# Kernel tuning notes

Measured on AMD Instinct MI355X. Metric: run time of the kernel, lower is better.

The kernel has to match this reference:

```python
import jax, jax.numpy as jnp
import numpy as np

NUM_HEADS = 8
QK_DIM = 64
V_DIM = 64


def _conv1x1(W, b, x):
    # W: [out, in], x: [N, in, T, V] -> [N, out, T, V]
    return jnp.einsum('oc,nctv->notv', W, x) + b[None, :, None, None]


def setup_inputs() -> dict:
    key = jax.random.key(0)
    ks = jax.random.split(key, 10)
    N, C, T, V = 8, 256, 1024, 25
    s = 0.02
    return {
        'feature': jax.random.normal(ks[0], (N, C, T, V), jnp.float32),
        'text_feature': jax.random.normal(ks[1], (1, 512, 1, V), jnp.float32),
        'Wq': jax.random.normal(ks[2], (NUM_HEADS * QK_DIM, 512), jnp.float32) * s,
        'bq': jax.random.normal(ks[3], (NUM_HEADS * QK_DIM,), jnp.float32) * s,
        'Wk': jax.random.normal(ks[4], (NUM_HEADS * QK_DIM, 512), jnp.float32) * s,
        'bk': jax.random.normal(ks[5], (NUM_HEADS * QK_DIM,), jnp.float32) * s,
        'Wv': jax.random.normal(ks[6], (V_DIM, C), jnp.float32) * s,
        'bv': jax.random.normal(ks[7], (V_DIM,), jnp.float32) * s,
        'Wo': jax.random.normal(ks[8], (C, NUM_HEADS * V_DIM), jnp.float32) * s,
        'bo': jax.random.normal(ks[9], (C,), jnp.float32) * s,
    }


def reference(feature, text_feature, Wq, bq, Wk, bk, Wv, bv, Wo, bo):
    N, C, T, V = feature.shape
    tf = jnp.broadcast_to(text_feature, (N, 512, 1, V))  # expand over batch
    # Q/K from text features (T dim collapses to 1)
    q = _conv1x1(Wq, bq, tf).reshape(N, NUM_HEADS, QK_DIM, V)
    k = _conv1x1(Wk, bk, tf).reshape(N, NUM_HEADS, QK_DIM, V)
    v = _conv1x1(Wv, bv, feature)  # [N, v_dim, T, V]
    energy = jnp.einsum('nhcu,nhcv->nhuv', q, k) / jnp.sqrt(jnp.float32(QK_DIM))
    attn = jax.nn.softmax(energy, axis=-1)  # [N, H, V, V]
    z = jnp.einsum('nctu,nhuv->nhctv', v, attn).reshape(N, NUM_HEADS * V_DIM, T, V)
    out = _conv1x1(Wo, bo, z) + feature
    return out
```

## Files before the change

kernel.cpp:

```cpp
#include <hip/hip_runtime.h>
#include <hip/hip_bf16.h>


typedef __attribute__((ext_vector_type(8))) short short8;
typedef __attribute__((ext_vector_type(4))) float f4v;

static __device__ __forceinline__ unsigned short f2bf(float f) {
  union { float f; unsigned u; } v; v.f = f;
  unsigned r = v.u + 0x7fffu + ((v.u >> 16) & 1u);
  return (unsigned short)(r >> 16);
}
static __device__ __forceinline__ float bf2f(unsigned short h) {
  union { unsigned u; float f; } v; v.u = ((unsigned)h) << 16;
  return v.f;
}


__global__ void k_qk_conv(const float* __restrict__ tf,
                          const float* __restrict__ Wq, const float* __restrict__ bq,
                          const float* __restrict__ Wk, const float* __restrict__ bk,
                          const float* __restrict__ Wv, const float* __restrict__ Wo,
                          unsigned short* __restrict__ WvP,
                          unsigned short* __restrict__ WoP,
                          float* __restrict__ qkP)
{
  __shared__ float tfl[12800];
  const int b = blockIdx.x, tid = threadIdx.x;
  if (b < 100) {
    for (int i = tid; i < 12800; i += 256) tfl[i] = tf[i];
    __syncthreads();
    int idx = b * 256 + tid;
    int isK = idx >= 12800;
    int j = isK ? idx - 12800 : idx;
    int g = j / 25, u = j - 25 * g;
    const float* wrow = (isK ? Wk : Wq) + g * 512;
    float s = (isK ? bk : bq)[g];
    for (int i = 0; i < 512; ++i) s += wrow[i] * tfl[i * 25 + u];
    qkP[idx] = s;
  } else {
    int cb = b - 100;
    for (int i = cb * 256 + tid; i < 16896; i += 64 * 256) {
      int c = i / 264, kk = i - 264 * c;
      WvP[i] = (kk < 256) ? f2bf(Wv[c * 256 + kk]) : (unsigned short)0;
    }
    for (int i = cb * 256 + tid; i < 147456; i += 64 * 256) {
      int hh = i / 18432, rr = i - 18432 * hh;
      int o = rr / 72, kk = rr - 72 * o;
      WoP[i] = (kk < 64) ? f2bf(Wo[o * 512 + hh * 64 + kk]) : (unsigned short)0;
    }
  }
}

__global__ void k_attn(const float* __restrict__ qkP,
                       unsigned short* __restrict__ attnP)
{
  __shared__ float ql[1600], kl[1600], attl[625];
  const int h = blockIdx.x, tid = threadIdx.x;
  for (int i = tid; i < 1600; i += 256) {
    ql[i] = qkP[h * 1600 + i];
    kl[i] = qkP[12800 + h * 1600 + i];
  }
  __syncthreads();
  if (tid < 25) {
    int u = tid;
    float e[25];
    float mx = -1e30f;
    #pragma unroll
    for (int v = 0; v < 25; ++v) {
      float s = 0.f;
      #pragma unroll
      for (int r = 0; r < 64; ++r) s += ql[r * 25 + u] * kl[r * 25 + v];
      s *= 0.125f;
      e[v] = s;
      mx = fmaxf(mx, s);
    }
    float den = 0.f;
    #pragma unroll
    for (int v = 0; v < 25; ++v) { e[v] = __expf(e[v] - mx); den += e[v]; }
    float inv = 1.f / den;
    #pragma unroll
    for (int v = 0; v < 25; ++v) attl[u * 25 + v] = e[v] * inv;
  }
  __syncthreads();
  for (int i = tid; i < 1280; i += 256) {
    int vp = i / 40, u = i - 40 * vp;
    attnP[h * 1280 + i] =
        (vp < 25 && u < 25) ? f2bf(attl[u * 25 + vp]) : (unsigned short)0;
  }
}

__launch_bounds__(512, 2)
__global__ void k_main(const float* __restrict__ feature,
                       const float* __restrict__ bv,
                       const float* __restrict__ bo,
                       const unsigned short* __restrict__ WvP,
                       const unsigned short* __restrict__ WoP,
                       const unsigned short* __restrict__ attnP,
                       float* __restrict__ out)
{
  extern __shared__ char smem[];
  unsigned short* Fl = (unsigned short*)smem;
  unsigned short* Vl = (unsigned short*)(smem + 67584);
  unsigned short* Zl = (unsigned short*)(smem + 84992);
  unsigned short* Wl = (unsigned short*)(smem + 103424);

  const int tid  = threadIdx.x;
  const int wave = tid >> 6;
  const int lane = tid & 63;
  const int quad = lane >> 4;
  const int l16  = lane & 15;
  const int n  = blockIdx.x >> 8;
  const int tb = blockIdx.x & 255;
  const int t0 = tb * 4;

  {
    short8 z = {0, 0, 0, 0, 0, 0, 0, 0};
    short8* fz = (short8*)smem;
    for (int i = tid; i < 4224; i += 512) fz[i] = z;
  }
  __syncthreads();

  {
    const int c = tid >> 1, p = tid & 1;
    const float4* src = reinterpret_cast<const float4*>(
        feature + ((size_t)(n * 256 + c) * 1024 + t0) * 25);
    for (int i = p; i < 25; i += 2) {
      float4 f = src[i];
      float vv[4] = {f.x, f.y, f.z, f.w};
      int j0 = 4 * i;
      #pragma unroll
      for (int e = 0; e < 4; ++e) {
        int j = j0 + e;
        int t = j / 25;
        int vp = j - 25 * t;
        Fl[(t * 32 + vp) * 264 + c] = f2bf(vv[e]);
      }
    }
  }
  __syncthreads();

  const int wm = wave >> 1, wn = wave & 1;

  f4v acc[4][4];
  #pragma unroll
  for (int mi = 0; mi < 4; ++mi) {
    #pragma unroll
    for (int r = 0; r < 4; ++r) {
      int o = wm * 64 + mi * 16 + quad * 4 + r;
      float bor = bo[o];
      #pragma unroll
      for (int ni = 0; ni < 4; ++ni) {
        int colb = wn * 64 + ni * 16 + l16;
        acc[mi][ni][r] = bor + bf2f(Fl[colb * 264 + o]);
      }
    }
  }

  {
    const int mt1 = wave & 3, nh1 = wave >> 2;
    f4v accv[4];
    #pragma unroll
    for (int ni = 0; ni < 4; ++ni) {
      #pragma unroll
      for (int r = 0; r < 4; ++r) accv[ni][r] = bv[mt1 * 16 + quad * 4 + r];
    }
    #pragma unroll
    for (int ks = 0; ks < 8; ++ks) {
      short8 a = *reinterpret_cast<const short8*>(
          WvP + (mt1 * 16 + l16) * 264 + ks * 32 + quad * 8);
      #pragma unroll
      for (int ni = 0; ni < 4; ++ni) {
        int colb = (4 * nh1 + ni) * 16 + l16;
        short8 b = *reinterpret_cast<const short8*>(
            &Fl[colb * 264 + ks * 32 + quad * 8]);
        accv[ni] = __builtin_amdgcn_mfma_f32_16x16x32_bf16(a, b, accv[ni], 0, 0, 0);
      }
    }
    #pragma unroll
    for (int ni = 0; ni < 4; ++ni) {
      int colb = (4 * nh1 + ni) * 16 + l16;
      #pragma unroll
      for (int r = 0; r < 4; ++r) {
        int c = mt1 * 16 + quad * 4 + r;
        Vl[c * 136 + colb] = f2bf(accv[ni][r]);
      }
    }
  }
  __syncthreads();

  #pragma unroll 1
  for (int h = 0; h < 8; ++h) {
    const short8* wsrc = reinterpret_cast<const short8*>(WoP + h * 18432);
    short8 wo_stage[5];
    #pragma unroll
    for (int c2 = 0; c2 < 5; ++c2) {
      int i = tid + c2 * 512;
      if (i < 2304) wo_stage[c2] = wsrc[i];
    }

    {
      const int t2 = wave >> 1, mh = wave & 1;
      f4v accz[2][2];
      #pragma unroll
      for (int m2 = 0; m2 < 2; ++m2) {
        #pragma unroll
        for (int n2 = 0; n2 < 2; ++n2) {
          f4v z = {0.f, 0.f, 0.f, 0.f};
          accz[m2][n2] = z;
        }
      }
      short8 bfrag[2];
      #pragma unroll
      for (int n2 = 0; n2 < 2; ++n2)
        bfrag[n2] = *reinterpret_cast<const short8*>(
            attnP + h * 1280 + (n2 * 16 + l16) * 40 + quad * 8);
      #pragma unroll
      for (int m2 = 0; m2 < 2; ++m2) {
        short8 a = *reinterpret_cast<const short8*>(
            &Vl[((2 * mh + m2) * 16 + l16) * 136 + t2 * 32 + quad * 8]);
        #pragma unroll
        for (int n2 = 0; n2 < 2; ++n2)
          accz[m2][n2] =
              __builtin_amdgcn_mfma_f32_16x16x32_bf16(a, bfrag[n2], accz[m2][n2], 0, 0, 0);
      }
      #pragma unroll
      for (int m2 = 0; m2 < 2; ++m2) {
        #pragma unroll
        for (int n2 = 0; n2 < 2; ++n2) {
          #pragma unroll
          for (int r = 0; r < 4; ++r) {
            int c = (2 * mh + m2) * 16 + quad * 4 + r;
            int colz = t2 * 32 + n2 * 16 + l16;
            Zl[colz * 72 + c] = f2bf(accz[m2][n2][r]);
          }
        }
      }
    }

    {
      short8* wdst = reinterpret_cast<short8*>(Wl);
      #pragma unroll
      for (int c2 = 0; c2 < 5; ++c2) {
        int i = tid + c2 * 512;
        if (i < 2304) wdst[i] = wo_stage[c2];
      }
    }
    __syncthreads();

    #pragma unroll
    for (int ks = 0; ks < 2; ++ks) {
      short8 afr[4], bfr[4];
      #pragma unroll
      for (int mi = 0; mi < 4; ++mi)
        afr[mi] = *reinterpret_cast<const short8*>(
            &Wl[(wm * 64 + mi * 16 + l16) * 72 + ks * 32 + quad * 8]);
      #pragma unroll
      for (int ni = 0; ni < 4; ++ni)
        bfr[ni] = *reinterpret_cast<const short8*>(
            &Zl[(wn * 64 + ni * 16 + l16) * 72 + ks * 32 + quad * 8]);
      #pragma unroll
      for (int mi = 0; mi < 4; ++mi) {
        #pragma unroll
        for (int ni = 0; ni < 4; ++ni)
          acc[mi][ni] =
              __builtin_amdgcn_mfma_f32_16x16x32_bf16(afr[mi], bfr[ni], acc[mi][ni], 0, 0, 0);
      }
    }
    __syncthreads();
  }

  #pragma unroll
  for (int ni = 0; ni < 4; ++ni) {
    int colb = wn * 64 + ni * 16 + l16;
    int t = colb >> 5, vp = colb & 31;
    if (vp < 25) {
      #pragma unroll
      for (int mi = 0; mi < 4; ++mi) {
        #pragma unroll
        for (int r = 0; r < 4; ++r) {
          int o = wm * 64 + mi * 16 + quad * 4 + r;
          out[((size_t)(n * 256 + o) * 1024 + (t0 + t)) * 25 + vp] = acc[mi][ni][r];
        }
      }
    }
  }
}

extern "C" void kernel_launch(void* const* d_in, const int* in_sizes, int n_in,
                              void* d_out, int out_size, void* d_ws, size_t ws_size,
                              hipStream_t stream)
{
  const float* feature = (const float*)d_in[0];
  const float* tf      = (const float*)d_in[1];
  const float* Wq      = (const float*)d_in[2];
  const float* bq      = (const float*)d_in[3];
  const float* Wk      = (const float*)d_in[4];
  const float* bk      = (const float*)d_in[5];
  const float* Wv      = (const float*)d_in[6];
  const float* bv      = (const float*)d_in[7];
  const float* Wo      = (const float*)d_in[8];
  const float* bo      = (const float*)d_in[9];
  float* out = (float*)d_out;

  unsigned short* WvP   = (unsigned short*)d_ws;
  unsigned short* WoP   = WvP + 16896;
  unsigned short* attnP = WoP + 147456;
  float* qkP = (float*)(attnP + 10240);

  hipLaunchKernelGGL(k_qk_conv, dim3(164), dim3(256), 0, stream,
                     tf, Wq, bq, Wk, bk, Wv, Wo, WvP, WoP, qkP);
  hipLaunchKernelGGL(k_attn, dim3(8), dim3(256), 0, stream, qkP, attnP);

  hipFuncSetAttribute(reinterpret_cast<const void*>(&k_main),
                      hipFuncAttributeMaxDynamicSharedMemorySize, 140288);
  hipLaunchKernelGGL(k_main, dim3(2048), dim3(512), 140288, stream,
                     feature, bv, bo, WvP, WoP, attnP, out);
}
```

Measured before the change: 549.8 us.

## Restructure main kernel to 2-timestep tiles with single-pass Wo GEMM

The main kernel now processes 2 timesteps per block instead of 4, cutting shared memory from about 140KB to 76KB so more blocks can be resident (launch bounds raised to 4). The per-head loop of Z-compute, Wo staging to LDS and barriers is replaced by one phase that computes all 8 heads' Z into a single LDS buffer, followed by one K=512 GEMM that reads Wo fragments directly from global memory. The preprocessing kernel is also reworked: the Q/K projection is computed with one wave per output row, the weights are bf16-converted with vectorized, unpadded copies, and the attention energy computation is spread across all threads. Reading Wo from global/L2 in the inner loop and using a smaller N tile per block may increase weight traffic.

```diff
diff --git a/kernel.cpp b/kernel.cpp
--- a/kernel.cpp
+++ b/kernel.cpp
@@ -3,6 +3,7 @@
 
 
 typedef __attribute__((ext_vector_type(8))) short short8;
+typedef __attribute__((ext_vector_type(4))) short short4v;
 typedef __attribute__((ext_vector_type(4))) float f4v;
 
 static __device__ __forceinline__ unsigned short f2bf(float f) {
@@ -16,37 +17,52 @@
 }
 
 
-__global__ void k_qk_conv(const float* __restrict__ tf,
-                          const float* __restrict__ Wq, const float* __restrict__ bq,
-                          const float* __restrict__ Wk, const float* __restrict__ bk,
-                          const float* __restrict__ Wv, const float* __restrict__ Wo,
-                          unsigned short* __restrict__ WvP,
-                          unsigned short* __restrict__ WoP,
-                          float* __restrict__ qkP)
-{
-  __shared__ float tfl[12800];
-  const int b = blockIdx.x, tid = threadIdx.x;
-  if (b < 100) {
-    for (int i = tid; i < 12800; i += 256) tfl[i] = tf[i];
-    __syncthreads();
-    int idx = b * 256 + tid;
-    int isK = idx >= 12800;
-    int j = isK ? idx - 12800 : idx;
-    int g = j / 25, u = j - 25 * g;
-    const float* wrow = (isK ? Wk : Wq) + g * 512;
-    float s = (isK ? bk : bq)[g];
-    for (int i = 0; i < 512; ++i) s += wrow[i] * tfl[i * 25 + u];
-    qkP[idx] = s;
+__global__ void k_pre(const float* __restrict__ tf,
+                      const float* __restrict__ Wq, const float* __restrict__ bq,
+                      const float* __restrict__ Wk, const float* __restrict__ bk,
+                      const float* __restrict__ Wv, const float* __restrict__ Wo,
+                      unsigned short* __restrict__ WvP,
+                      unsigned short* __restrict__ WoP,
+                      float* __restrict__ qkP)
+{
+  const int bx = blockIdx.x, tid = threadIdx.x;
+  if (bx < 256) {
+    const int r = __builtin_amdgcn_readfirstlane(bx * 4 + (tid >> 6));
+    const int u = tid & 63;
+    const int u2 = (u < 25) ? u : 24;
+    const int isK = r >= 512, g = r & 511;
+    const float* W = (isK ? Wk : Wq) + g * 512;
+    float s0 = 0.f, s1 = 0.f, s2 = 0.f, s3 = 0.f;
+    #pragma unroll 4
+    for (int i = 0; i < 512; i += 4) {
+      s0 += W[i + 0] * tf[(i + 0) * 25 + u2];
+      s1 += W[i + 1] * tf[(i + 1) * 25 + u2];
+      s2 += W[i + 2] * tf[(i + 2) * 25 + u2];
+      s3 += W[i + 3] * tf[(i + 3) * 25 + u2];
+    }
+    float s = ((s0 + s1) + (s2 + s3)) + (isK ? bk : bq)[g];
+    if (u < 25) qkP[r * 25 + u] = s;
+  } else if (bx < 288) {
+    const float4* W4 = reinterpret_cast<const float4*>(Wo);
+    short4v* D4 = reinterpret_cast<short4v*>(WoP);
+    int base = (bx - 256) * 256 + tid;
+    #pragma unroll
+    for (int e = 0; e < 4; ++e) {
+      int i4 = base + e * 8192;
+      float4 f = W4[i4];
+      short4v s = {(short)f2bf(f.x), (short)f2bf(f.y), (short)f2bf(f.z), (short)f2bf(f.w)};
+      D4[i4] = s;
+    }
   } else {
-    int cb = b - 100;
-    for (int i = cb * 256 + tid; i < 16896; i += 64 * 256) {
-      int c = i / 264, kk = i - 264 * c;
-      WvP[i] = (kk < 256) ? f2bf(Wv[c * 256 + kk]) : (unsigned short)0;
-    }
-    for (int i = cb * 256 + tid; i < 147456; i += 64 * 256) {
-      int hh = i / 18432, rr = i - 18432 * hh;
-      int o = rr / 72, kk = rr - 72 * o;
-      WoP[i] = (kk < 64) ? f2bf(Wo[o * 512 + hh * 64 + kk]) : (unsigned short)0;
+    const float4* W4 = reinterpret_cast<const float4*>(Wv);
+    short4v* D4 = reinterpret_cast<short4v*>(WvP);
+    int base = (bx - 288) * 256 + tid;
+    #pragma unroll
+    for (int e = 0; e < 8; ++e) {
+      int i4 = base + e * 512;
+      float4 f = W4[i4];
+      short4v s = {(short)f2bf(f.x), (short)f2bf(f.y), (short)f2bf(f.z), (short)f2bf(f.w)};
+      D4[i4] = s;
     }
   }
 }
@@ -54,42 +70,43 @@
 __global__ void k_attn(const float* __restrict__ qkP,
                        unsigned short* __restrict__ attnP)
 {
-  __shared__ float ql[1600], kl[1600], attl[625];
+  __shared__ float ql[1600], kl[1600], el[625];
   const int h = blockIdx.x, tid = threadIdx.x;
   for (int i = tid; i < 1600; i += 256) {
     ql[i] = qkP[h * 1600 + i];
     kl[i] = qkP[12800 + h * 1600 + i];
   }
   __syncthreads();
+  for (int p = tid; p < 625; p += 256) {
+    int u = p / 25, v = p - 25 * u;
+    float s = 0.f;
+    #pragma unroll 16
+    for (int c = 0; c < 64; ++c) s += ql[c * 25 + u] * kl[c * 25 + v];
+    el[p] = s * 0.125f;
+  }
+  __syncthreads();
   if (tid < 25) {
-    int u = tid;
-    float e[25];
+    const int u = tid;
     float mx = -1e30f;
     #pragma unroll
-    for (int v = 0; v < 25; ++v) {
-      float s = 0.f;
-      #pragma unroll
-      for (int r = 0; r < 64; ++r) s += ql[r * 25 + u] * kl[r * 25 + v];
-      s *= 0.125f;
-      e[v] = s;
-      mx = fmaxf(mx, s);
-    }
+    for (int v = 0; v < 25; ++v) mx = fmaxf(mx, el[u * 25 + v]);
     float den = 0.f;
-    #pragma unroll
-    for (int v = 0; v < 25; ++v) { e[v] = __expf(e[v] - mx); den += e[v]; }
+    float ex[25];
+    #pragma unroll
+    for (int v = 0; v < 25; ++v) { ex[v] = __expf(el[u * 25 + v] - mx); den += ex[v]; }
     float inv = 1.f / den;
     #pragma unroll
-    for (int v = 0; v < 25; ++v) attl[u * 25 + v] = e[v] * inv;
+    for (int v = 0; v < 25; ++v) el[u * 25 + v] = ex[v] * inv;
   }
   __syncthreads();
   for (int i = tid; i < 1280; i += 256) {
-    int vp = i / 40, u = i - 40 * vp;
+    int vp = i / 40, uu = i - 40 * vp;
     attnP[h * 1280 + i] =
-        (vp < 25 && u < 25) ? f2bf(attl[u * 25 + vp]) : (unsigned short)0;
-  }
-}
-
-__launch_bounds__(512, 2)
+        (vp < 25 && uu < 25) ? f2bf(el[uu * 25 + vp]) : (unsigned short)0;
+  }
+}
+
+__launch_bounds__(512, 4)
 __global__ void k_main(const float* __restrict__ feature,
                        const float* __restrict__ bv,
                        const float* __restrict__ bo,
@@ -100,185 +117,131 @@
 {
   extern __shared__ char smem[];
   unsigned short* Fl = (unsigned short*)smem;
-  unsigned short* Vl = (unsigned short*)(smem + 67584);
-  unsigned short* Zl = (unsigned short*)(smem + 84992);
-  unsigned short* Wl = (unsigned short*)(smem + 103424);
+  unsigned short* Za = (unsigned short*)smem;
+  unsigned short* Vl = (unsigned short*)(smem + 66560);
 
   const int tid  = threadIdx.x;
   const int wave = tid >> 6;
   const int lane = tid & 63;
   const int quad = lane >> 4;
   const int l16  = lane & 15;
-  const int n  = blockIdx.x >> 8;
-  const int tb = blockIdx.x & 255;
-  const int t0 = tb * 4;
-
-  {
-    short8 z = {0, 0, 0, 0, 0, 0, 0, 0};
-    short8* fz = (short8*)smem;
-    for (int i = tid; i < 4224; i += 512) fz[i] = z;
-  }
-  __syncthreads();
+  const int n  = blockIdx.x >> 9;
+  const int tb = blockIdx.x & 511;
+  const int t0 = tb * 2;
 
   {
     const int c = tid >> 1, p = tid & 1;
-    const float4* src = reinterpret_cast<const float4*>(
+    const float2* src = reinterpret_cast<const float2*>(
         feature + ((size_t)(n * 256 + c) * 1024 + t0) * 25);
     for (int i = p; i < 25; i += 2) {
-      float4 f = src[i];
-      float vv[4] = {f.x, f.y, f.z, f.w};
-      int j0 = 4 * i;
-      #pragma unroll
-      for (int e = 0; e < 4; ++e) {
-        int j = j0 + e;
-        int t = j / 25;
-        int vp = j - 25 * t;
-        Fl[(t * 32 + vp) * 264 + c] = f2bf(vv[e]);
-      }
-    }
-  }
-  __syncthreads();
-
-  const int wm = wave >> 1, wn = wave & 1;
-
-  f4v acc[4][4];
-  #pragma unroll
-  for (int mi = 0; mi < 4; ++mi) {
-    #pragma unroll
-    for (int r = 0; r < 4; ++r) {
-      int o = wm * 64 + mi * 16 + quad * 4 + r;
-      float bor = bo[o];
-      #pragma unroll
-      for (int ni = 0; ni < 4; ++ni) {
-        int colb = wn * 64 + ni * 16 + l16;
-        acc[mi][ni][r] = bor + bf2f(Fl[colb * 264 + o]);
-      }
-    }
-  }
-
-  {
-    const int mt1 = wave & 3, nh1 = wave >> 2;
-    f4v accv[4];
-    #pragma unroll
-    for (int ni = 0; ni < 4; ++ni) {
-      #pragma unroll
-      for (int r = 0; r < 4; ++r) accv[ni][r] = bv[mt1 * 16 + quad * 4 + r];
-    }
-    #pragma unroll
+      float2 f = src[i];
+      int j = 2 * i;
+      int t = (j >= 25); int vp = j - 25 * t;
+      Fl[(t * 32 + vp) * 264 + c] = f2bf(f.x);
+      ++j; t = (j >= 25); vp = j - 25 * t;
+      Fl[(t * 32 + vp) * 264 + c] = f2bf(f.y);
+    }
+    #pragma unroll
+    for (int z = p; z < 14; z += 2) {
+      int t = (z >= 7); int vp = 25 + z - 7 * t;
+      Fl[(t * 32 + vp) * 264 + c] = 0;
+    }
+  }
+  __syncthreads();
+
+  {
+    const int mt = wave & 3, nh = wave >> 2;
+    f4v accv[2];
+    #pragma unroll
+    for (int ni = 0; ni < 2; ++ni)
+      #pragma unroll
+      for (int r = 0; r < 4; ++r) accv[ni][r] = bv[mt * 16 + quad * 4 + r];
+    #pragma unroll 2
     for (int ks = 0; ks < 8; ++ks) {
       short8 a = *reinterpret_cast<const short8*>(
-          WvP + (mt1 * 16 + l16) * 264 + ks * 32 + quad * 8);
-      #pragma unroll
-      for (int ni = 0; ni < 4; ++ni) {
-        int colb = (4 * nh1 + ni) * 16 + l16;
+          WvP + (mt * 16 + l16) * 256 + ks * 32 + quad * 8);
+      #pragma unroll
+      for (int ni = 0; ni < 2; ++ni) {
         short8 b = *reinterpret_cast<const short8*>(
-            &Fl[colb * 264 + ks * 32 + quad * 8]);
+            &Fl[(nh * 32 + ni * 16 + l16) * 264 + ks * 32 + quad * 8]);
         accv[ni] = __builtin_amdgcn_mfma_f32_16x16x32_bf16(a, b, accv[ni], 0, 0, 0);
       }
     }
     #pragma unroll
-    for (int ni = 0; ni < 4; ++ni) {
-      int colb = (4 * nh1 + ni) * 16 + l16;
-      #pragma unroll
-      for (int r = 0; r < 4; ++r) {
-        int c = mt1 * 16 + quad * 4 + r;
-        Vl[c * 136 + colb] = f2bf(accv[ni][r]);
+    for (int ni = 0; ni < 2; ++ni)
+      #pragma unroll
+      for (int r = 0; r < 4; ++r)
+        Vl[(mt * 16 + quad * 4 + r) * 72 + nh * 32 + ni * 16 + l16] =
+            f2bf(accv[ni][r]);
+  }
+
+  f4v acc[2][4];
+  #pragma unroll
+  for (int mi = 0; mi < 2; ++mi) {
+    #pragma unroll
+    for (int r = 0; r < 4; ++r) {
+      int o = wave * 32 + mi * 16 + quad * 4 + r;
+      float bor = bo[o];
+      #pragma unroll
+      for (int ni = 0; ni < 4; ++ni)
+        acc[mi][ni][r] = bor + bf2f(Fl[(ni * 16 + l16) * 264 + o]);
+    }
+  }
+  __syncthreads();
+
+  {
+    const int h = wave;
+    short8 bfr2[2];
+    bfr2[0] = *reinterpret_cast<const short8*>(attnP + h * 1280 + l16 * 40 + quad * 8);
+    bfr2[1] = *reinterpret_cast<const short8*>(attnP + h * 1280 + (16 + l16) * 40 + quad * 8);
+    #pragma unroll
+    for (int nt = 0; nt < 4; ++nt) {
+      int t = nt >> 1, vh = nt & 1;
+      #pragma unroll
+      for (int mi = 0; mi < 4; ++mi) {
+        f4v az = {0.f, 0.f, 0.f, 0.f};
+        short8 a = *reinterpret_cast<const short8*>(
+            &Vl[(mi * 16 + l16) * 72 + t * 32 + quad * 8]);
+        az = __builtin_amdgcn_mfma_f32_16x16x32_bf16(a, bfr2[vh], az, 0, 0, 0);
+        short4v pk = {(short)f2bf(az[0]), (short)f2bf(az[1]),
+                      (short)f2bf(az[2]), (short)f2bf(az[3])};
+        *reinterpret_cast<short4v*>(
+            &Za[(nt * 16 + l16) * 520 + h * 64 + mi * 16 + quad * 4]) = pk;
       }
     }
   }
   __syncthreads();
 
-  #pragma unroll 1
-  for (int h = 0; h < 8; ++h) {
-    const short8* wsrc = reinterpret_cast<const short8*>(WoP + h * 18432);
-    short8 wo_stage[5];
-    #pragma unroll
-    for (int c2 = 0; c2 < 5; ++c2) {
-      int i = tid + c2 * 512;
-      if (i < 2304) wo_stage[c2] = wsrc[i];
-    }
-
-    {
-      const int t2 = wave >> 1, mh = wave & 1;
-      f4v accz[2][2];
-      #pragma unroll
-      for (int m2 = 0; m2 < 2; ++m2) {
-        #pragma unroll
-        for (int n2 = 0; n2 < 2; ++n2) {
-          f4v z = {0.f, 0.f, 0.f, 0.f};
-          accz[m2][n2] = z;
-        }
-      }
-      short8 bfrag[2];
-      #pragma unroll
-      for (int n2 = 0; n2 < 2; ++n2)
-        bfrag[n2] = *reinterpret_cast<const short8*>(
-            attnP + h * 1280 + (n2 * 16 + l16) * 40 + quad * 8);
-      #pragma unroll
-      for (int m2 = 0; m2 < 2; ++m2) {
-        short8 a = *reinterpret_cast<const short8*>(
-            &Vl[((2 * mh + m2) * 16 + l16) * 136 + t2 * 32 + quad * 8]);
-        #pragma unroll
-        for (int n2 = 0; n2 < 2; ++n2)
-          accz[m2][n2] =
-              __builtin_amdgcn_mfma_f32_16x16x32_bf16(a, bfrag[n2], accz[m2][n2], 0, 0, 0);
-      }
-      #pragma unroll
-      for (int m2 = 0; m2 < 2; ++m2) {
-        #pragma unroll
-        for (int n2 = 0; n2 < 2; ++n2) {
-          #pragma unroll
-          for (int r = 0; r < 4; ++r) {
-            int c = (2 * mh + m2) * 16 + quad * 4 + r;
-            int colz = t2 * 32 + n2 * 16 + l16;
-            Zl[colz * 72 + c] = f2bf(accz[m2][n2][r]);
-          }
-        }
-      }
-    }
-
-    {
-      short8* wdst = reinterpret_cast<short8*>(Wl);
-      #pragma unroll
-      for (int c2 = 0; c2 < 5; ++c2) {
-        int i = tid + c2 * 512;
-        if (i < 2304) wdst[i] = wo_stage[c2];
-      }
-    }
-    __syncthreads();
-
-    #pragma unroll
-    for (int ks = 0; ks < 2; ++ks) {
-      short8 afr[4], bfr[4];
-      #pragma unroll
-      for (int mi = 0; mi < 4; ++mi)
-        afr[mi] = *reinterpret_cast<const short8*>(
-            &Wl[(wm * 64 + mi * 16 + l16) * 72 + ks * 32 + quad * 8]);
-      #pragma unroll
-      for (int ni = 0; ni < 4; ++ni)
-        bfr[ni] = *reinterpret_cast<const short8*>(
-            &Zl[(wn * 64 + ni * 16 + l16) * 72 + ks * 32 + quad * 8]);
-      #pragma unroll
-      for (int mi = 0; mi < 4; ++mi) {
-        #pragma unroll
-        for (int ni = 0; ni < 4; ++ni)
-          acc[mi][ni] =
-              __builtin_amdgcn_mfma_f32_16x16x32_bf16(afr[mi], bfr[ni], acc[mi][ni], 0, 0, 0);
-      }
-    }
-    __syncthreads();
+  {
+    const unsigned short* wbase = WoP + ((size_t)(wave * 32 + l16)) * 512;
+    #pragma unroll 2
+    for (int ks = 0; ks < 16; ++ks) {
+      short8 a0 = *reinterpret_cast<const short8*>(wbase + ks * 32 + quad * 8);
+      short8 a1 = *reinterpret_cast<const short8*>(wbase + 16 * 512 + ks * 32 + quad * 8);
+      short8 b[4];
+      #pragma unroll
+      for (int ni = 0; ni < 4; ++ni)
+        b[ni] = *reinterpret_cast<const short8*>(
+            &Za[(ni * 16 + l16) * 520 + ks * 32 + quad * 8]);
+      #pragma unroll
+      for (int ni = 0; ni < 4; ++ni)
+        acc[0][ni] = __builtin_amdgcn_mfma_f32_16x16x32_bf16(a0, b[ni], acc[0][ni], 0, 0, 0);
+      #pragma unroll
+      for (int ni = 0; ni < 4; ++ni)
+        acc[1][ni] = __builtin_amdgcn_mfma_f32_16x16x32_bf16(a1, b[ni], acc[1][ni], 0, 0, 0);
+    }
   }
 
   #pragma unroll
   for (int ni = 0; ni < 4; ++ni) {
-    int colb = wn * 64 + ni * 16 + l16;
-    int t = colb >> 5, vp = colb & 31;
+    int col = ni * 16 + l16;
+    int t = col >> 5, vp = col & 31;
     if (vp < 25) {
       #pragma unroll
-      for (int mi = 0; mi < 4; ++mi) {
+      for (int mi = 0; mi < 2; ++mi) {
         #pragma unroll
         for (int r = 0; r < 4; ++r) {
-          int o = wm * 64 + mi * 16 + quad * 4 + r;
+          int o = wave * 32 + mi * 16 + quad * 4 + r;
           out[((size_t)(n * 256 + o) * 1024 + (t0 + t)) * 25 + vp] = acc[mi][ni][r];
         }
       }
@@ -303,16 +266,16 @@
   float* out = (float*)d_out;
 
   unsigned short* WvP   = (unsigned short*)d_ws;
-  unsigned short* WoP   = WvP + 16896;
-  unsigned short* attnP = WoP + 147456;
+  unsigned short* WoP   = WvP + 16384;
+  unsigned short* attnP = WoP + 131072;
   float* qkP = (float*)(attnP + 10240);
 
-  hipLaunchKernelGGL(k_qk_conv, dim3(164), dim3(256), 0, stream,
+  hipLaunchKernelGGL(k_pre, dim3(290), dim3(256), 0, stream,
                      tf, Wq, bq, Wk, bk, Wv, Wo, WvP, WoP, qkP);
   hipLaunchKernelGGL(k_attn, dim3(8), dim3(256), 0, stream, qkP, attnP);
 
   hipFuncSetAttribute(reinterpret_cast<const void*>(&k_main),
-                      hipFuncAttributeMaxDynamicSharedMemorySize, 140288);
-  hipLaunchKernelGGL(k_main, dim3(2048), dim3(512), 140288, stream,
+                      hipFuncAttributeMaxDynamicSharedMemorySize, 75776);
+  hipLaunchKernelGGL(k_main, dim3(4096), dim3(512), 75776, stream,
                      feature, bv, bo, WvP, WoP, attnP, out);
 }
```

Result: slower. 569.7 us (+3.6%).
